# Performance work log

Hardware: AMD Instinct MI355X
Metric: run time of the kernel (lower is better)

The kernel has to match this reference:

```python
import jax, jax.numpy as jnp
import numpy as np

NUM_HEADS = 12
HEAD_SIZE = 64
HIDDEN = 768


def setup_inputs() -> dict:
    key = jax.random.key(0)
    ks = jax.random.split(key, 5)
    B, S, H = 2, 2048, HIDDEN
    scale_in = 0.02
    return {
        "x": jax.random.normal(ks[0], (B, S, H), dtype=jnp.float32),
        "w_qkv": jax.random.normal(ks[1], (3 * H, H), dtype=jnp.float32) * scale_in,
        "b_qkv": jax.random.normal(ks[2], (3 * H,), dtype=jnp.float32) * scale_in,
        "w_o": jax.random.normal(ks[3], (H, H), dtype=jnp.float32) * scale_in,
        "b_o": jax.random.normal(ks[4], (H,), dtype=jnp.float32) * scale_in,
    }


def reference(x, w_qkv, b_qkv, w_o, b_o):
    B, S, H = x.shape
    nh, hd = NUM_HEADS, HEAD_SIZE
    qkv = x @ w_qkv.T + b_qkv                      # (B, S, 3H)
    Q, K, V = jnp.split(qkv, 3, axis=-1)
    Q = Q.reshape(B, S, nh, hd)
    K = K.reshape(B, S, nh, hd)
    V = V.reshape(B, S, nh, hd)
    # scores: (B, nh, S_q, S_k)
    scores = jnp.einsum('bqhd,bkhd->bhqk', Q, K)
    causal = jnp.triu(jnp.ones((S, S), dtype=bool), k=1)
    scores = jnp.where(causal, -jnp.inf, scores)
    attn = jax.nn.softmax(scores / jnp.sqrt(jnp.float32(hd)), axis=3)
    out = jnp.einsum('bhqk,bkhd->bqhd', attn, V).reshape(B, S, nh * hd)
    return out @ w_o.T + b_o
```

## Files before the change

kernel.cpp:

```cpp
#include <hip/hip_runtime.h>
#include <stdint.h>


#define B_   2
#define S_   2048
#define H_   768
#define NH_  12
#define HD_  64
#define M_   4096
#define K_   768
#define N_QKV 2304
#define QKV_ELEMS (B_*NH_*S_*HD_)
#define SCL_ 0.18033688f

using bf16x8 = __attribute__((ext_vector_type(8))) __bf16;
using f32x4  = __attribute__((ext_vector_type(4))) float;
using f32x16 = __attribute__((ext_vector_type(16))) float;

__device__ inline unsigned short f2bf(float f) {
  unsigned int u = __float_as_uint(f);
  u = (u + 0x7FFFu + ((u >> 16) & 1u)) >> 16;
  return (unsigned short)u;
}
__device__ inline float fexp2(float x) {
  float r; asm("v_exp_f32 %0, %1" : "=v"(r) : "v"(x)); return r;
}
__device__ inline unsigned cvtpk(float lo, float hi) {
  unsigned r; asm("v_cvt_pk_bf16_f32 %0, %1, %2" : "=v"(r) : "v"(lo), "v"(hi)); return r;
}
__device__ inline void gload_lds16(const void* g, void* l) {
  __builtin_amdgcn_global_load_lds((const __attribute__((address_space(1))) void*)g,
                                   (__attribute__((address_space(3))) void*)l, 16, 0, 0);
}
#define VWAIT0() do { asm volatile("s_waitcnt vmcnt(0)" ::: "memory"); \
                      __builtin_amdgcn_sched_barrier(0); } while (0)
#define LWAIT0() do { asm volatile("s_waitcnt lgkmcnt(0)" ::: "memory"); \
                      __builtin_amdgcn_sched_barrier(0); } while (0)

__global__ void cast3(const float* __restrict__ s0, unsigned short* __restrict__ d0, int n0f,
                      const float* __restrict__ s1, unsigned short* __restrict__ d1, int n1f,
                      const float* __restrict__ s2, unsigned short* __restrict__ d2, int n2f) {
  int i = blockIdx.x * blockDim.x + threadIdx.x;
  const float* s; unsigned short* d; int j;
  if (i < n0f)                { s = s0; d = d0; j = i; }
  else if (i < n0f + n1f)     { s = s1; d = d1; j = i - n0f; }
  else if (i < n0f + n1f + n2f) { s = s2; d = d2; j = i - n0f - n1f; }
  else return;
  float4 v = reinterpret_cast<const float4*>(s)[j];
  ushort4 o;
  o.x = f2bf(v.x); o.y = f2bf(v.y); o.z = f2bf(v.z); o.w = f2bf(v.w);
  reinterpret_cast<ushort4*>(d)[j] = o;
}

template<int N, int MODE, int GX>
__global__ __launch_bounds__(256, 3)
void gemm_nt(const unsigned short* __restrict__ A,
             const unsigned short* __restrict__ Bw,
             const float* __restrict__ bias,
             unsigned short* __restrict__ qkv_base,
             float* __restrict__ outp)
{
  __shared__ unsigned short As[128*64];
  __shared__ unsigned short Bs[128*64];
  const int tid  = threadIdx.x;
  const int lane = tid & 63;
  const int wid  = tid >> 6;
  const int g = lane >> 4, lr = lane & 15;
  const int wm = wid >> 1, wn = wid & 1;
  const int cpx = (GX * 32) >> 3;
  const int id  = blockIdx.x;
  const int sw  = (id & 7) * cpx + (id >> 3);
  const int n0 = (sw % GX) * 128;
  const int m0 = (sw / GX) * 128;

  f32x4 acc[4][4];
  #pragma unroll
  for (int i = 0; i < 4; ++i)
    #pragma unroll
    for (int j = 0; j < 4; ++j) acc[i][j] = f32x4{0.f, 0.f, 0.f, 0.f};

  for (int k0 = 0; k0 < K_; k0 += 64) {
    #pragma unroll
    for (int it = 0; it < 4; ++it) {
      int c = it*256 + wid*64 + lane;
      int row = c >> 3, seg = (c & 7) ^ (row & 7);
      int lb = __builtin_amdgcn_readfirstlane((it*256 + wid*64) * 8);
      gload_lds16(&A [(size_t)(m0 + row) * K_ + k0 + seg*8], &As[lb]);
      gload_lds16(&Bw[(size_t)(n0 + row) * K_ + k0 + seg*8], &Bs[lb]);
    }
    __syncthreads();
    #pragma unroll
    for (int ks = 0; ks < 2; ++ks) {
      bf16x8 af[4], bfr[4];
      #pragma unroll
      for (int i = 0; i < 4; ++i) {
        int ra = wm*64 + i*16 + lr;
        af[i]  = *reinterpret_cast<const bf16x8*>(&As[(ra*8 + ((ks*4+g) ^ (ra&7)))*8]);
        int rb = wn*64 + i*16 + lr;
        bfr[i] = *reinterpret_cast<const bf16x8*>(&Bs[(rb*8 + ((ks*4+g) ^ (rb&7)))*8]);
      }
      #pragma unroll
      for (int i = 0; i < 4; ++i)
        #pragma unroll
        for (int j = 0; j < 4; ++j)
          acc[i][j] = __builtin_amdgcn_mfma_f32_16x16x32_bf16(af[i], bfr[j], acc[i][j], 0, 0, 0);
    }
    __syncthreads();
  }

  #pragma unroll
  for (int j = 0; j < 4; ++j) {
    int col = n0 + wn*64 + j*16 + lr;
    float bv = bias[col];
    if constexpr (MODE == 0) {
      int which = col / 768;
      int rem = col - which * 768;
      int h = rem >> 6, d = rem & 63;
      if (which == 0) {
        unsigned short* dst = qkv_base;
        #pragma unroll
        for (int i = 0; i < 4; ++i)
          #pragma unroll
          for (int r = 0; r < 4; ++r) {
            int rowm = m0 + wm*64 + i*16 + g*4 + r;
            int bb = rowm >> 11, ss = rowm & 2047;
            dst[(((size_t)(bb*NH_ + h))*S_ + ss)*HD_ + d] = f2bf(acc[i][j][r] + bv);
          }
      } else if (which == 1) {
        unsigned short* dst = qkv_base + (size_t)QKV_ELEMS;
        #pragma unroll
        for (int i = 0; i < 4; ++i)
          #pragma unroll
          for (int r = 0; r < 4; ++r) {
            int rowm = m0 + wm*64 + i*16 + g*4 + r;
            int bb = rowm >> 11, ss = rowm & 2047;
            size_t byteoff = ((size_t)(bb*NH_ + h)*(S_>>5) + (ss>>5))*4096
                           + (size_t)(((d>>3)*32 + (ss&31))*16 + (d&7)*2);
            dst[byteoff >> 1] = f2bf(acc[i][j][r] + bv);
          }
      } else {
        unsigned short* dst = qkv_base + 2*(size_t)QKV_ELEMS;
        #pragma unroll
        for (int i = 0; i < 4; ++i) {
          int rowm = m0 + wm*64 + i*16 + g*4;
          int bb = rowm >> 11, ss = rowm & 2047;
          unsigned w0 = (unsigned)f2bf(acc[i][j][0] + bv) | ((unsigned)f2bf(acc[i][j][1] + bv) << 16);
          unsigned w1 = (unsigned)f2bf(acc[i][j][2] + bv) | ((unsigned)f2bf(acc[i][j][3] + bv) << 16);
          uint2 u; u.x = w0; u.y = w1;
          size_t byteoff = ((size_t)(bb*NH_ + h)*(S_>>5) + (ss>>5))*4096
                         + (size_t)((((ss&31)>>3)*64 + d)*16 + (ss&7)*2);
          *reinterpret_cast<uint2*>(&dst[byteoff >> 1]) = u;
        }
      }
    } else {
      #pragma unroll
      for (int i = 0; i < 4; ++i)
        #pragma unroll
        for (int r = 0; r < 4; ++r) {
          int rowm = m0 + wm*64 + i*16 + g*4 + r;
          outp[(size_t)rowm * H_ + col] = acc[i][j][r] + bv;
        }
    }
  }
}

__global__ __launch_bounds__(256, 2)
void attn_fwd(const unsigned short* __restrict__ Qp,
              const unsigned short* __restrict__ Ktp,
              const unsigned short* __restrict__ Vtp,
              unsigned short* __restrict__ attn)
{
  __shared__ __align__(16) char smem[34816];
  float* mlb = (float*)(smem + 32768);

  const int tid = threadIdx.x;
  const int l = tid & 63, w = tid >> 6;
  const int q31 = l & 31, hi = l >> 5;
  const int idx = blockIdx.x;
  const int bh = (idx & 7) + 8 * ((idx >> 3) % 3);
  const int pr = (idx >> 3) / 3;
  const unsigned short* Qh = Qp + (size_t)bh * S_ * HD_;
  const char* Ktb = (const char*)Ktp + (size_t)bh * (S_>>5) * 4096;
  const char* Vtb = (const char*)Vtp + (size_t)bh * (S_>>5) * 4096;
  const int bb = bh / NH_, hh = bh % NH_;

  unsigned short* Kl = (unsigned short*)(smem + w*8192);
  unsigned short* Vl = Kl + 2048;
  float* OscW = (float*)(smem + w*8192);

  const int qtH = 63 - pr, qtL = pr;
  const int qrowH = qtH*32 + q31, qrowL = qtL*32 + q31;

  bf16x8 qfH[4], qfL[4];
  #pragma unroll
  for (int ks = 0; ks < 4; ++ks) {
    qfH[ks] = *reinterpret_cast<const bf16x8*>(&Qh[(size_t)qrowH*HD_ + ks*16 + hi*8]);
    qfL[ks] = *reinterpret_cast<const bf16x8*>(&Qh[(size_t)qrowL*HD_ + ks*16 + hi*8]);
  }

  f32x16 oH0, oH1, oL0, oL1;
  #pragma unroll
  for (int r = 0; r < 16; ++r) { oH0[r]=0.f; oH1[r]=0.f; oL0[r]=0.f; oL1[r]=0.f; }
  float lrunH = 0.f, lrunL = 0.f;

  const int p = w;
  const int ntH = ((qtH - p) >> 2) + 1;
  const int ntL = (qtL >= p) ? ((qtL - p) >> 2) + 1 : 0;
  const bool dwH = ((qtH & 3) == p);
  const bool dwL = ((qtL & 3) == p);
  const int ntHm1 = ntH - 1, ntLm1 = ntL - 1;

  const char* kt = Ktb + (size_t)p*4096 + l*16;
  const char* vt = Vtb + (size_t)p*4096 + l*16;

  auto STAGE = [&]() {
    gload_lds16(kt,        Kl);
    gload_lds16(kt + 1024, Kl + 512);
    gload_lds16(kt + 2048, Kl + 1024);
    gload_lds16(kt + 3072, Kl + 1536);
    gload_lds16(vt,        Vl);
    gload_lds16(vt + 1024, Vl + 512);
    gload_lds16(vt + 2048, Vl + 1024);
    gload_lds16(vt + 3072, Vl + 1536);
    kt += 16384; vt += 16384;
  };

  STAGE();

  for (int i = 0; i < ntH; ++i) {
    VWAIT0();
    bf16x8 k0 = *reinterpret_cast<const bf16x8*>(&Kl[((0+hi)*32 + q31)*8]);
    bf16x8 k1 = *reinterpret_cast<const bf16x8*>(&Kl[((2+hi)*32 + q31)*8]);
    bf16x8 k2 = *reinterpret_cast<const bf16x8*>(&Kl[((4+hi)*32 + q31)*8]);
    bf16x8 k3 = *reinterpret_cast<const bf16x8*>(&Kl[((6+hi)*32 + q31)*8]);
    bf16x8 v0 = *reinterpret_cast<const bf16x8*>(&Vl[((  hi)*64 +      q31)*8]);
    bf16x8 v1 = *reinterpret_cast<const bf16x8*>(&Vl[((2+hi)*64 +      q31)*8]);
    bf16x8 v2 = *reinterpret_cast<const bf16x8*>(&Vl[((  hi)*64 + 32 + q31)*8]);
    bf16x8 v3 = *reinterpret_cast<const bf16x8*>(&Vl[((2+hi)*64 + 32 + q31)*8]);
    LWAIT0();
    if (i + 1 < ntH) STAGE();
    asm volatile("" ::: "memory");

    const bool doL = (i < ntL);

    f32x16 sfH;
    #pragma unroll
    for (int r = 0; r < 16; ++r) sfH[r] = 0.f;
    sfH = __builtin_amdgcn_mfma_f32_32x32x16_bf16(k0, qfH[0], sfH, 0, 0, 0);
    sfH = __builtin_amdgcn_mfma_f32_32x32x16_bf16(k1, qfH[1], sfH, 0, 0, 0);
    sfH = __builtin_amdgcn_mfma_f32_32x32x16_bf16(k2, qfH[2], sfH, 0, 0, 0);
    sfH = __builtin_amdgcn_mfma_f32_32x32x16_bf16(k3, qfH[3], sfH, 0, 0, 0);
    f32x16 sfL;
    #pragma unroll
    for (int r = 0; r < 16; ++r) sfL[r] = 0.f;
    if (doL) {
      sfL = __builtin_amdgcn_mfma_f32_32x32x16_bf16(k0, qfL[0], sfL, 0, 0, 0);
      sfL = __builtin_amdgcn_mfma_f32_32x32x16_bf16(k1, qfL[1], sfL, 0, 0, 0);
      sfL = __builtin_amdgcn_mfma_f32_32x32x16_bf16(k2, qfL[2], sfL, 0, 0, 0);
      sfL = __builtin_amdgcn_mfma_f32_32x32x16_bf16(k3, qfL[3], sfL, 0, 0, 0);
    }

    if (dwH && i == ntHm1) {
      const int kv0 = qtH*32;
      #pragma unroll
      for (int r = 0; r < 16; ++r) {
        int kv = kv0 + (r & 3) + 8*(r >> 2) + 4*hi;
        if (kv > qrowH) sfH[r] = -1e38f;
      }
    }
    if (doL && dwL && i == ntLm1) {
      const int kv0 = qtL*32;
      #pragma unroll
      for (int r = 0; r < 16; ++r) {
        int kv = kv0 + (r & 3) + 8*(r >> 2) + 4*hi;
        if (kv > qrowL) sfL[r] = -1e38f;
      }
    }

    #pragma unroll
    for (int r = 0; r < 16; ++r) sfH[r] = fexp2(sfH[r] * SCL_);
    {
      float s0 = (sfH[0]+sfH[1])+(sfH[2]+sfH[3]);
      float s1 = (sfH[4]+sfH[5])+(sfH[6]+sfH[7]);
      float s2 = (sfH[8]+sfH[9])+(sfH[10]+sfH[11]);
      float s3 = (sfH[12]+sfH[13])+(sfH[14]+sfH[15]);
      lrunH += (s0+s1)+(s2+s3);
      unsigned pw0 = cvtpk(sfH[0],sfH[1]),  pw1 = cvtpk(sfH[2],sfH[3]);
      unsigned pw2 = cvtpk(sfH[4],sfH[5]),  pw3 = cvtpk(sfH[6],sfH[7]);
      unsigned pw4 = cvtpk(sfH[8],sfH[9]),  pw5 = cvtpk(sfH[10],sfH[11]);
      unsigned pw6 = cvtpk(sfH[12],sfH[13]), pw7 = cvtpk(sfH[14],sfH[15]);
      asm("v_permlane32_swap_b32 %0, %1" : "+v"(pw0), "+v"(pw2));
      asm("v_permlane32_swap_b32 %0, %1" : "+v"(pw1), "+v"(pw3));
      asm("v_permlane32_swap_b32 %0, %1" : "+v"(pw4), "+v"(pw6));
      asm("v_permlane32_swap_b32 %0, %1" : "+v"(pw5), "+v"(pw7));
      uint4 pf0; pf0.x = pw0; pf0.y = pw1; pf0.z = pw2; pf0.w = pw3;
      uint4 pf1; pf1.x = pw4; pf1.y = pw5; pf1.z = pw6; pf1.w = pw7;
      oH0 = __builtin_amdgcn_mfma_f32_32x32x16_bf16(v0, *reinterpret_cast<bf16x8*>(&pf0), oH0, 0, 0, 0);
      oH0 = __builtin_amdgcn_mfma_f32_32x32x16_bf16(v1, *reinterpret_cast<bf16x8*>(&pf1), oH0, 0, 0, 0);
      oH1 = __builtin_amdgcn_mfma_f32_32x32x16_bf16(v2, *reinterpret_cast<bf16x8*>(&pf0), oH1, 0, 0, 0);
      oH1 = __builtin_amdgcn_mfma_f32_32x32x16_bf16(v3, *reinterpret_cast<bf16x8*>(&pf1), oH1, 0, 0, 0);
    }

    if (doL) {
      #pragma unroll
      for (int r = 0; r < 16; ++r) sfL[r] = fexp2(sfL[r] * SCL_);
      float s0 = (sfL[0]+sfL[1])+(sfL[2]+sfL[3]);
      float s1 = (sfL[4]+sfL[5])+(sfL[6]+sfL[7]);
      float s2 = (sfL[8]+sfL[9])+(sfL[10]+sfL[11]);
      float s3 = (sfL[12]+sfL[13])+(sfL[14]+sfL[15]);
      lrunL += (s0+s1)+(s2+s3);
      unsigned pw0 = cvtpk(sfL[0],sfL[1]),  pw1 = cvtpk(sfL[2],sfL[3]);
      unsigned pw2 = cvtpk(sfL[4],sfL[5]),  pw3 = cvtpk(sfL[6],sfL[7]);
      unsigned pw4 = cvtpk(sfL[8],sfL[9]),  pw5 = cvtpk(sfL[10],sfL[11]);
      unsigned pw6 = cvtpk(sfL[12],sfL[13]), pw7 = cvtpk(sfL[14],sfL[15]);
      asm("v_permlane32_swap_b32 %0, %1" : "+v"(pw0), "+v"(pw2));
      asm("v_permlane32_swap_b32 %0, %1" : "+v"(pw1), "+v"(pw3));
      asm("v_permlane32_swap_b32 %0, %1" : "+v"(pw4), "+v"(pw6));
      asm("v_permlane32_swap_b32 %0, %1" : "+v"(pw5), "+v"(pw7));
      uint4 pf0; pf0.x = pw0; pf0.y = pw1; pf0.z = pw2; pf0.w = pw3;
      uint4 pf1; pf1.x = pw4; pf1.y = pw5; pf1.z = pw6; pf1.w = pw7;
      oL0 = __builtin_amdgcn_mfma_f32_32x32x16_bf16(v0, *reinterpret_cast<bf16x8*>(&pf0), oL0, 0, 0, 0);
      oL0 = __builtin_amdgcn_mfma_f32_32x32x16_bf16(v1, *reinterpret_cast<bf16x8*>(&pf1), oL0, 0, 0, 0);
      oL1 = __builtin_amdgcn_mfma_f32_32x32x16_bf16(v2, *reinterpret_cast<bf16x8*>(&pf0), oL1, 0, 0, 0);
      oL1 = __builtin_amdgcn_mfma_f32_32x32x16_bf16(v3, *reinterpret_cast<bf16x8*>(&pf1), oL1, 0, 0, 0);
    }
  }

  const int q = tid & 31, dseg8 = tid >> 5;

  auto MERGE = [&](const f32x16& a0v, const f32x16& a1v, float lr, int qt) {
    __syncthreads();
    #pragma unroll
    for (int rr = 0; rr < 4; ++rr) {
      f32x4 a;
      #pragma unroll
      for (int e = 0; e < 4; ++e) a[e] = a0v[4*rr + e];
      *reinterpret_cast<f32x4*>(&OscW[q31*36 + 8*rr + 4*hi]) = a;
    }
    mlb[w*64 + hi*32 + q31] = lr;
    __syncthreads();
    float inv;
    {
      float lt = (mlb[q] + mlb[32+q]) + (mlb[64+q] + mlb[96+q])
               + (mlb[128+q] + mlb[160+q]) + (mlb[192+q] + mlb[224+q]);
      inv = 1.f / lt;
    }
    if (dseg8 < 4) {
      const int dd = dseg8*8;
      #define OSC(a, off) (*reinterpret_cast<f32x4*>((float*)(smem + (a)*8192) + (off)))
      f32x4 a0 = OSC(0, q*36 + dd), b0 = OSC(0, q*36 + dd + 4);
      f32x4 a1 = OSC(1, q*36 + dd), b1 = OSC(1, q*36 + dd + 4);
      f32x4 a2 = OSC(2, q*36 + dd), b2 = OSC(2, q*36 + dd + 4);
      f32x4 a3 = OSC(3, q*36 + dd), b3 = OSC(3, q*36 + dd + 4);
      f32x4 ra, rb;
      #pragma unroll
      for (int e = 0; e < 4; ++e) {
        ra[e] = ((a0[e] + a1[e]) + (a2[e] + a3[e])) * inv;
        rb[e] = ((b0[e] + b1[e]) + (b2[e] + b3[e])) * inv;
      }
      uint4 ov;
      ov.x = cvtpk(ra[0], ra[1]); ov.y = cvtpk(ra[2], ra[3]);
      ov.z = cvtpk(rb[0], rb[1]); ov.w = cvtpk(rb[2], rb[3]);
      *reinterpret_cast<uint4*>(&attn[((size_t)(bb*S_ + qt*32 + q))*H_ + hh*HD_ + dd]) = ov;
    }
    __syncthreads();
    #pragma unroll
    for (int rr = 0; rr < 4; ++rr) {
      f32x4 a;
      #pragma unroll
      for (int e = 0; e < 4; ++e) a[e] = a1v[4*rr + e];
      *reinterpret_cast<f32x4*>(&OscW[q31*36 + 8*rr + 4*hi]) = a;
    }
    __syncthreads();
    if (dseg8 >= 4) {
      const int dd = (dseg8 - 4)*8;
      f32x4 a0 = OSC(0, q*36 + dd), b0 = OSC(0, q*36 + dd + 4);
      f32x4 a1 = OSC(1, q*36 + dd), b1 = OSC(1, q*36 + dd + 4);
      f32x4 a2 = OSC(2, q*36 + dd), b2 = OSC(2, q*36 + dd + 4);
      f32x4 a3 = OSC(3, q*36 + dd), b3 = OSC(3, q*36 + dd + 4);
      #undef OSC
      f32x4 ra, rb;
      #pragma unroll
      for (int e = 0; e < 4; ++e) {
        ra[e] = ((a0[e] + a1[e]) + (a2[e] + a3[e])) * inv;
        rb[e] = ((b0[e] + b1[e]) + (b2[e] + b3[e])) * inv;
      }
      uint4 ov;
      ov.x = cvtpk(ra[0], ra[1]); ov.y = cvtpk(ra[2], ra[3]);
      ov.z = cvtpk(rb[0], rb[1]); ov.w = cvtpk(rb[2], rb[3]);
      *reinterpret_cast<uint4*>(&attn[((size_t)(bb*S_ + qt*32 + q))*H_ + hh*HD_ + 32 + dd]) = ov;
    }
    __syncthreads();
  };

  MERGE(oH0, oH1, lrunH, qtH);
  MERGE(oL0, oL1, lrunL, qtL);
}

extern "C" void kernel_launch(void* const* d_in, const int* in_sizes, int n_in,
                              void* d_out, int out_size, void* d_ws, size_t ws_size,
                              hipStream_t stream)
{
  const float* x      = (const float*)d_in[0];
  const float* w_qkv  = (const float*)d_in[1];
  const float* b_qkv  = (const float*)d_in[2];
  const float* w_o    = (const float*)d_in[3];
  const float* b_o    = (const float*)d_in[4];
  float* out = (float*)d_out;

  unsigned short* xb    = (unsigned short*)d_ws;
  unsigned short* wqkvb = xb    + (size_t)M_ * K_;
  unsigned short* wob   = wqkvb + (size_t)N_QKV * K_;
  unsigned short* Qw    = wob   + (size_t)H_ * H_;
  unsigned short* Ktw   = Qw + (size_t)QKV_ELEMS;
  unsigned short* Vtw   = Ktw + (size_t)QKV_ELEMS;
  unsigned short* attn  = Vtw + (size_t)QKV_ELEMS;

  cast3<<<5376, 256, 0, stream>>>(x, xb, 786432,
                                  w_qkv, wqkvb, 442368,
                                  w_o, wob, 147456);
  gemm_nt<N_QKV, 0, 18><<<576, 256, 0, stream>>>(xb, wqkvb, b_qkv, Qw, nullptr);
  attn_fwd<<<dim3(768), 256, 0, stream>>>(Qw, Ktw, Vtw, attn);
  gemm_nt<H_, 1, 6><<<192, 256, 0, stream>>>(attn, wob, b_o, nullptr, out);
}
```

Measured before the change: 72.40 us.

## Double-buffer K/V staging in attention and use 64-row tiles for output GEMM

The attention kernel now gives each wave two LDS buffers for K/V tiles and prefetches two tiles ahead. It waits with vmcnt(8), so the next tile's global loads overlap compute on the current tile. The output projection GEMM is templated on the M tile size and launched with 64-row tiles and 384 blocks, so more of the GPU is filled for the small N=768 GEMM. The cost is doubled LDS per attention block (about 65KB), which may lower occupancy. The smaller GEMM tile also gives less reuse of the loaded B tile.

```diff
diff --git a/kernel.cpp b/kernel.cpp
--- a/kernel.cpp
+++ b/kernel.cpp
@@ -33,6 +33,8 @@
                                    (__attribute__((address_space(3))) void*)l, 16, 0, 0);
 }
 #define VWAIT0() do { asm volatile("s_waitcnt vmcnt(0)" ::: "memory"); \
+                      __builtin_amdgcn_sched_barrier(0); } while (0)
+#define VWAIT8() do { asm volatile("s_waitcnt vmcnt(8)" ::: "memory"); \
                       __builtin_amdgcn_sched_barrier(0); } while (0)
 #define LWAIT0() do { asm volatile("s_waitcnt lgkmcnt(0)" ::: "memory"); \
                       __builtin_amdgcn_sched_barrier(0); } while (0)
@@ -52,7 +54,7 @@
   reinterpret_cast<ushort4*>(d)[j] = o;
 }
 
-template<int N, int MODE, int GX>
+template<int N, int MODE, int GX, int TM>
 __global__ __launch_bounds__(256, 3)
 void gemm_nt(const unsigned short* __restrict__ A,
              const unsigned short* __restrict__ Bw,
@@ -60,47 +62,57 @@
              unsigned short* __restrict__ qkv_base,
              float* __restrict__ outp)
 {
-  __shared__ unsigned short As[128*64];
+  __shared__ unsigned short As[TM*64];
   __shared__ unsigned short Bs[128*64];
   const int tid  = threadIdx.x;
   const int lane = tid & 63;
   const int wid  = tid >> 6;
   const int g = lane >> 4, lr = lane & 15;
   const int wm = wid >> 1, wn = wid & 1;
-  const int cpx = (GX * 32) >> 3;
+  const int cpx = (GX * (M_/TM)) >> 3;
   const int id  = blockIdx.x;
   const int sw  = (id & 7) * cpx + (id >> 3);
   const int n0 = (sw % GX) * 128;
-  const int m0 = (sw / GX) * 128;
-
-  f32x4 acc[4][4];
+  const int m0 = (sw / GX) * TM;
+  constexpr int NI = TM / 32;
+
+  f32x4 acc[NI][4];
   #pragma unroll
-  for (int i = 0; i < 4; ++i)
+  for (int i = 0; i < NI; ++i)
     #pragma unroll
     for (int j = 0; j < 4; ++j) acc[i][j] = f32x4{0.f, 0.f, 0.f, 0.f};
 
   for (int k0 = 0; k0 < K_; k0 += 64) {
+    #pragma unroll
+    for (int it = 0; it < TM/32; ++it) {
+      int c = it*256 + wid*64 + lane;
+      int row = c >> 3, seg = (c & 7) ^ (row & 7);
+      int lb = __builtin_amdgcn_readfirstlane((it*256 + wid*64) * 8);
+      gload_lds16(&A[(size_t)(m0 + row) * K_ + k0 + seg*8], &As[lb]);
+    }
     #pragma unroll
     for (int it = 0; it < 4; ++it) {
       int c = it*256 + wid*64 + lane;
       int row = c >> 3, seg = (c & 7) ^ (row & 7);
       int lb = __builtin_amdgcn_readfirstlane((it*256 + wid*64) * 8);
-      gload_lds16(&A [(size_t)(m0 + row) * K_ + k0 + seg*8], &As[lb]);
       gload_lds16(&Bw[(size_t)(n0 + row) * K_ + k0 + seg*8], &Bs[lb]);
     }
     __syncthreads();
     #pragma unroll
     for (int ks = 0; ks < 2; ++ks) {
-      bf16x8 af[4], bfr[4];
-      #pragma unroll
-      for (int i = 0; i < 4; ++i) {
-        int ra = wm*64 + i*16 + lr;
+      bf16x8 af[NI], bfr[4];
+      #pragma unroll
+      for (int i = 0; i < NI; ++i) {
+        int ra = wm*(TM/2) + i*16 + lr;
         af[i]  = *reinterpret_cast<const bf16x8*>(&As[(ra*8 + ((ks*4+g) ^ (ra&7)))*8]);
-        int rb = wn*64 + i*16 + lr;
-        bfr[i] = *reinterpret_cast<const bf16x8*>(&Bs[(rb*8 + ((ks*4+g) ^ (rb&7)))*8]);
-      }
-      #pragma unroll
-      for (int i = 0; i < 4; ++i)
+      }
+      #pragma unroll
+      for (int j = 0; j < 4; ++j) {
+        int rb = wn*64 + j*16 + lr;
+        bfr[j] = *reinterpret_cast<const bf16x8*>(&Bs[(rb*8 + ((ks*4+g) ^ (rb&7)))*8]);
+      }
+      #pragma unroll
+      for (int i = 0; i < NI; ++i)
         #pragma unroll
         for (int j = 0; j < 4; ++j)
           acc[i][j] = __builtin_amdgcn_mfma_f32_16x16x32_bf16(af[i], bfr[j], acc[i][j], 0, 0, 0);
@@ -119,20 +131,20 @@
       if (which == 0) {
         unsigned short* dst = qkv_base;
         #pragma unroll
-        for (int i = 0; i < 4; ++i)
+        for (int i = 0; i < NI; ++i)
           #pragma unroll
           for (int r = 0; r < 4; ++r) {
-            int rowm = m0 + wm*64 + i*16 + g*4 + r;
+            int rowm = m0 + wm*(TM/2) + i*16 + g*4 + r;
             int bb = rowm >> 11, ss = rowm & 2047;
             dst[(((size_t)(bb*NH_ + h))*S_ + ss)*HD_ + d] = f2bf(acc[i][j][r] + bv);
           }
       } else if (which == 1) {
         unsigned short* dst = qkv_base + (size_t)QKV_ELEMS;
         #pragma unroll
-        for (int i = 0; i < 4; ++i)
+        for (int i = 0; i < NI; ++i)
           #pragma unroll
           for (int r = 0; r < 4; ++r) {
-            int rowm = m0 + wm*64 + i*16 + g*4 + r;
+            int rowm = m0 + wm*(TM/2) + i*16 + g*4 + r;
             int bb = rowm >> 11, ss = rowm & 2047;
             size_t byteoff = ((size_t)(bb*NH_ + h)*(S_>>5) + (ss>>5))*4096
                            + (size_t)(((d>>3)*32 + (ss&31))*16 + (d&7)*2);
@@ -141,8 +153,8 @@
       } else {
         unsigned short* dst = qkv_base + 2*(size_t)QKV_ELEMS;
         #pragma unroll
-        for (int i = 0; i < 4; ++i) {
-          int rowm = m0 + wm*64 + i*16 + g*4;
+        for (int i = 0; i < NI; ++i) {
+          int rowm = m0 + wm*(TM/2) + i*16 + g*4;
           int bb = rowm >> 11, ss = rowm & 2047;
           unsigned w0 = (unsigned)f2bf(acc[i][j][0] + bv) | ((unsigned)f2bf(acc[i][j][1] + bv) << 16);
           unsigned w1 = (unsigned)f2bf(acc[i][j][2] + bv) | ((unsigned)f2bf(acc[i][j][3] + bv) << 16);
@@ -154,10 +166,10 @@
       }
     } else {
       #pragma unroll
-      for (int i = 0; i < 4; ++i)
+      for (int i = 0; i < NI; ++i)
         #pragma unroll
         for (int r = 0; r < 4; ++r) {
-          int rowm = m0 + wm*64 + i*16 + g*4 + r;
+          int rowm = m0 + wm*(TM/2) + i*16 + g*4 + r;
           outp[(size_t)rowm * H_ + col] = acc[i][j][r] + bv;
         }
     }
@@ -170,8 +182,8 @@
               const unsigned short* __restrict__ Vtp,
               unsigned short* __restrict__ attn)
 {
-  __shared__ __align__(16) char smem[34816];
-  float* mlb = (float*)(smem + 32768);
+  __shared__ __align__(16) char smem[66560];
+  float* mlb = (float*)(smem + 65536);
 
   const int tid = threadIdx.x;
   const int l = tid & 63, w = tid >> 6;
@@ -184,9 +196,7 @@
   const char* Vtb = (const char*)Vtp + (size_t)bh * (S_>>5) * 4096;
   const int bb = bh / NH_, hh = bh % NH_;
 
-  unsigned short* Kl = (unsigned short*)(smem + w*8192);
-  unsigned short* Vl = Kl + 2048;
-  float* OscW = (float*)(smem + w*8192);
+  float* OscW = (float*)(smem + w*16384);
 
   const int qtH = 63 - pr, qtL = pr;
   const int qrowH = qtH*32 + q31, qrowL = qtL*32 + q31;
@@ -197,6 +207,7 @@
     qfH[ks] = *reinterpret_cast<const bf16x8*>(&Qh[(size_t)qrowH*HD_ + ks*16 + hi*8]);
     qfL[ks] = *reinterpret_cast<const bf16x8*>(&Qh[(size_t)qrowL*HD_ + ks*16 + hi*8]);
   }
+  VWAIT0();
 
   f32x16 oH0, oH1, oL0, oL1;
   #pragma unroll
@@ -213,22 +224,27 @@
   const char* kt = Ktb + (size_t)p*4096 + l*16;
   const char* vt = Vtb + (size_t)p*4096 + l*16;
 
-  auto STAGE = [&]() {
-    gload_lds16(kt,        Kl);
-    gload_lds16(kt + 1024, Kl + 512);
-    gload_lds16(kt + 2048, Kl + 1024);
-    gload_lds16(kt + 3072, Kl + 1536);
-    gload_lds16(vt,        Vl);
-    gload_lds16(vt + 1024, Vl + 512);
-    gload_lds16(vt + 2048, Vl + 1024);
-    gload_lds16(vt + 3072, Vl + 1536);
+  auto STAGE = [&](int buf) {
+    unsigned short* Kb = (unsigned short*)(smem + w*16384 + buf*8192);
+    unsigned short* Vb = Kb + 2048;
+    gload_lds16(kt,        Kb);
+    gload_lds16(kt + 1024, Kb + 512);
+    gload_lds16(kt + 2048, Kb + 1024);
+    gload_lds16(kt + 3072, Kb + 1536);
+    gload_lds16(vt,        Vb);
+    gload_lds16(vt + 1024, Vb + 512);
+    gload_lds16(vt + 2048, Vb + 1024);
+    gload_lds16(vt + 3072, Vb + 1536);
     kt += 16384; vt += 16384;
   };
 
-  STAGE();
+  STAGE(0);
+  if (ntH > 1) STAGE(1);
 
   for (int i = 0; i < ntH; ++i) {
-    VWAIT0();
+    if (i == ntHm1) { VWAIT0(); } else { VWAIT8(); }
+    unsigned short* Kl = (unsigned short*)(smem + w*16384 + (i & 1)*8192);
+    unsigned short* Vl = Kl + 2048;
     bf16x8 k0 = *reinterpret_cast<const bf16x8*>(&Kl[((0+hi)*32 + q31)*8]);
     bf16x8 k1 = *reinterpret_cast<const bf16x8*>(&Kl[((2+hi)*32 + q31)*8]);
     bf16x8 k2 = *reinterpret_cast<const bf16x8*>(&Kl[((4+hi)*32 + q31)*8]);
@@ -238,7 +254,7 @@
     bf16x8 v2 = *reinterpret_cast<const bf16x8*>(&Vl[((  hi)*64 + 32 + q31)*8]);
     bf16x8 v3 = *reinterpret_cast<const bf16x8*>(&Vl[((2+hi)*64 + 32 + q31)*8]);
     LWAIT0();
-    if (i + 1 < ntH) STAGE();
+    if (i + 2 < ntH) STAGE(i & 1);
     asm volatile("" ::: "memory");
 
     const bool doL = (i < ntL);
@@ -347,7 +363,7 @@
     }
     if (dseg8 < 4) {
       const int dd = dseg8*8;
-      #define OSC(a, off) (*reinterpret_cast<f32x4*>((float*)(smem + (a)*8192) + (off)))
+      #define OSC(a, off) (*reinterpret_cast<f32x4*>((float*)(smem + (a)*16384) + (off)))
       f32x4 a0 = OSC(0, q*36 + dd), b0 = OSC(0, q*36 + dd + 4);
       f32x4 a1 = OSC(1, q*36 + dd), b1 = OSC(1, q*36 + dd + 4);
       f32x4 a2 = OSC(2, q*36 + dd), b2 = OSC(2, q*36 + dd + 4);
@@ -419,7 +435,7 @@
   cast3<<<5376, 256, 0, stream>>>(x, xb, 786432,
                                   w_qkv, wqkvb, 442368,
                                   w_o, wob, 147456);
-  gemm_nt<N_QKV, 0, 18><<<576, 256, 0, stream>>>(xb, wqkvb, b_qkv, Qw, nullptr);
+  gemm_nt<N_QKV, 0, 18, 128><<<576, 256, 0, stream>>>(xb, wqkvb, b_qkv, Qw, nullptr);
   attn_fwd<<<dim3(768), 256, 0, stream>>>(Qw, Ktw, Vtw, attn);
-  gemm_nt<H_, 1, 6><<<192, 256, 0, stream>>>(attn, wob, b_o, nullptr, out);
-}
+  gemm_nt<H_, 1, 6, 64><<<384, 256, 0, stream>>>(attn, wob, b_o, nullptr, out);
+}
```

Result: no change. 71.06 us (-1.9%).
